# Kernel optimization log

Measured on AMD Instinct MI355X. Metric: run time of the kernel, lower is better.

## Reference

```python
import jax, jax.numpy as jnp
import numpy as np

K_TOP = 16
NUM_HEADS = 12
EPS = 1e-6


def setup_inputs() -> dict:
    key = jax.random.key(0)
    ks = jax.random.split(key, 5)
    B, N, C = 4, 1024, 768
    scale = 0.02
    return {
        "x": jax.random.normal(ks[0], (B, N, C), dtype=jnp.float32),
        "in_proj_weight": jax.random.normal(ks[1], (3 * C, C), dtype=jnp.float32) * scale,
        "in_proj_bias": jax.random.normal(ks[2], (3 * C,), dtype=jnp.float32) * scale,
        "out_proj_weight": jax.random.normal(ks[3], (C, C), dtype=jnp.float32) * scale,
        "out_proj_bias": jax.random.normal(ks[4], (C,), dtype=jnp.float32) * scale,
    }


def reference(x, in_proj_weight, in_proj_bias, out_proj_weight, out_proj_bias):
    B, N, C = x.shape
    H = NUM_HEADS
    Dh = C // H
    scale = Dh ** (-0.5)
    # fused QKV projection: (B,N,3C) -> (3,B,H,N,Dh)
    qkv = x @ in_proj_weight.T + in_proj_bias
    qkv = qkv.reshape(B, N, 3, H, Dh).transpose(2, 0, 3, 1, 4)
    q, k, v = qkv[0], qkv[1], qkv[2]
    # dense scaled-dot-product scores, softmax over keys
    attn = jax.nn.softmax(jnp.einsum("bhqd,bhkd->bhqk", q, k) * scale, axis=-1)
    # top-k sparsification: keep k largest probs per query row, zero the rest
    topk_vals, topk_idx = jax.lax.top_k(attn, K_TOP)  # [B,H,N,K]
    bi = jnp.arange(B)[:, None, None, None]
    hi = jnp.arange(H)[None, :, None, None]
    ni = jnp.arange(N)[None, None, :, None]
    topk_attn = jnp.zeros_like(attn).at[bi, hi, ni, topk_idx].set(topk_vals)
    # renormalize surviving mass
    den = jnp.clip(topk_attn.sum(axis=-1, keepdims=True), EPS, None)
    topk_attn = topk_attn / den
    # weighted value aggregation + output projection
    x_out = jnp.einsum("bhqk,bhkd->bhqd", topk_attn, v)
    x_out = x_out.transpose(0, 2, 1, 3).reshape(B, N, C)
    x_out = x_out @ out_proj_weight.T + out_proj_bias
    return (x_out, topk_attn)
```

## Files before the change

### kernel.cpp

```cpp
#include <hip/hip_runtime.h>
#include <math.h>
#include <stdint.h>

#define BB 4
#define NN 1024
#define CC 768
#define HH 12
#define DH 64
#define KTOP 16

#define GATE     2e-4f
#define SUPERSET 4e-4f

typedef __attribute__((ext_vector_type(8))) short short8v;
typedef __attribute__((ext_vector_type(4))) short short4v;
typedef __attribute__((ext_vector_type(4))) float f32x4;

__device__ __forceinline__ short2 bf16split(float f) {
    uint32_t u = __float_as_uint(f);
    uint32_t hb = (u + 0x8000u) & 0xFFFF0000u;
    float hf = __uint_as_float(hb);
    float lo = f - hf;
    short2 r;
    r.x = (short)(hb >> 16);
    r.y = (short)((__float_as_uint(lo) + 0x8000u) >> 16);
    return r;
}

__device__ __forceinline__ short8v lds_load8(const short* p) {
    short4v a = *(const short4v*)p;
    short4v b = *(const short4v*)(p + 4);
    short8v r;
    r[0] = a[0]; r[1] = a[1]; r[2] = a[2]; r[3] = a[3];
    r[4] = b[0]; r[5] = b[1]; r[6] = b[2]; r[7] = b[3];
    return r;
}

__global__ __launch_bounds__(256) void qkv_mfma(
    const float* __restrict__ x, const float* __restrict__ w,
    const float* __restrict__ bias,
    short* __restrict__ qh_g, short* __restrict__ ql_g,
    short* __restrict__ kh_g, short* __restrict__ kl_g,
    float* __restrict__ v32, int* __restrict__ wl_count) {
    __shared__ short xh[128][36], xl[128][36];
    __shared__ short wh[64][36],  wl[64][36];
    const int tid = threadIdx.x;
    const int m0 = blockIdx.x * 128, n0 = blockIdx.y * 64;
    const int wave = tid >> 6, lane = tid & 63;
    const int wr = wave >> 1, wc = wave & 1;
    const int lr = lane & 15, lg = lane >> 4;

    if (blockIdx.x == 0 && blockIdx.y == 0 && tid == 0) *wl_count = 0;

    f32x4 acc[4][2];
#pragma unroll
    for (int i = 0; i < 4; ++i)
#pragma unroll
        for (int j = 0; j < 2; ++j) acc[i][j] = (f32x4)0.0f;

    for (int k0 = 0; k0 < CC; k0 += 32) {
        __syncthreads();
#pragma unroll
        for (int it = 0; it < 4; ++it) {
            int e = tid + 256 * it;
            int row = e >> 3, c4 = e & 7;
            float4 f = *reinterpret_cast<const float4*>(&x[(size_t)(m0 + row) * CC + k0 + 4 * c4]);
            short4v hv, lv;
            short2 s0 = bf16split(f.x); short2 s1 = bf16split(f.y);
            short2 s2 = bf16split(f.z); short2 s3 = bf16split(f.w);
            hv[0] = s0.x; lv[0] = s0.y; hv[1] = s1.x; lv[1] = s1.y;
            hv[2] = s2.x; lv[2] = s2.y; hv[3] = s3.x; lv[3] = s3.y;
            *(short4v*)&xh[row][4 * c4] = hv;
            *(short4v*)&xl[row][4 * c4] = lv;
        }
#pragma unroll
        for (int it = 0; it < 2; ++it) {
            int e = tid + 256 * it;
            int row = e >> 3, c4 = e & 7;
            float4 f = *reinterpret_cast<const float4*>(&w[(size_t)(n0 + row) * CC + k0 + 4 * c4]);
            short4v hv, lv;
            short2 s0 = bf16split(f.x); short2 s1 = bf16split(f.y);
            short2 s2 = bf16split(f.z); short2 s3 = bf16split(f.w);
            hv[0] = s0.x; lv[0] = s0.y; hv[1] = s1.x; lv[1] = s1.y;
            hv[2] = s2.x; lv[2] = s2.y; hv[3] = s3.x; lv[3] = s3.y;
            *(short4v*)&wh[row][4 * c4] = hv;
            *(short4v*)&wl[row][4 * c4] = lv;
        }
        __syncthreads();

        short8v ah[4], al[4], bh[2], bl[2];
#pragma unroll
        for (int mt = 0; mt < 4; ++mt) {
            int row = wr * 64 + mt * 16 + lr;
            ah[mt] = lds_load8(&xh[row][lg * 8]);
            al[mt] = lds_load8(&xl[row][lg * 8]);
        }
#pragma unroll
        for (int nt = 0; nt < 2; ++nt) {
            int col = wc * 32 + nt * 16 + lr;
            bh[nt] = lds_load8(&wh[col][lg * 8]);
            bl[nt] = lds_load8(&wl[col][lg * 8]);
        }
#pragma unroll
        for (int mt = 0; mt < 4; ++mt) {
#pragma unroll
            for (int nt = 0; nt < 2; ++nt) {
                acc[mt][nt] = __builtin_amdgcn_mfma_f32_16x16x32_bf16(ah[mt], bh[nt], acc[mt][nt], 0, 0, 0);
                acc[mt][nt] = __builtin_amdgcn_mfma_f32_16x16x32_bf16(ah[mt], bl[nt], acc[mt][nt], 0, 0, 0);
                acc[mt][nt] = __builtin_amdgcn_mfma_f32_16x16x32_bf16(al[mt], bh[nt], acc[mt][nt], 0, 0, 0);
            }
        }
    }

    const int t = n0 / CC;
#pragma unroll
    for (int mt = 0; mt < 4; ++mt) {
#pragma unroll
        for (int nt = 0; nt < 2; ++nt) {
#pragma unroll
            for (int r = 0; r < 4; ++r) {
                int m = m0 + wr * 64 + mt * 16 + lg * 4 + r;
                int col = n0 + wc * 32 + nt * 16 + lr;
                float val = acc[mt][nt][r] + bias[col];
                int rem = col - t * CC;
                int h = rem >> 6, d = rem & 63;
                int b = m >> 10, n = m & 1023;
                size_t off = (((size_t)(b * HH + h)) * NN + n) * DH + d;
                if (t == 0) {
                    short2 s = bf16split(val * 0.125f);
                    qh_g[off] = s.x; ql_g[off] = s.y;
                } else if (t == 1) {
                    short2 s = bf16split(val);
                    kh_g[off] = s.x; kl_g[off] = s.y;
                } else {
                    v32[off] = val;
                }
            }
        }
    }
}

__global__ __launch_bounds__(256) void scores_mfma(
    const short* __restrict__ qh_g, const short* __restrict__ ql_g,
    const short* __restrict__ kh_g, const short* __restrict__ kl_g,
    float* __restrict__ attn_out) {
    __shared__ short qh[64][68], ql[64][68];
    __shared__ short kh[128][68], kl[128][68];
    const int bh = blockIdx.y;
    const int m0 = blockIdx.x * 64;
    const int tid = threadIdx.x;
    const int wave = tid >> 6, lane = tid & 63;
    const int lr = lane & 15, lg = lane >> 4;

    const size_t qbase = ((size_t)bh * NN + m0) * DH;
    const size_t kbase = (size_t)bh * NN * DH;

#pragma unroll
    for (int it = 0; it < 2; ++it) {
        int e = tid + 256 * it;
        int row = e >> 3, c8 = (e & 7) << 3;
        size_t g = qbase + (size_t)row * DH + c8;
        *(short4v*)&qh[row][c8]     = *(const short4v*)&qh_g[g];
        *(short4v*)&qh[row][c8 + 4] = *(const short4v*)&qh_g[g + 4];
        *(short4v*)&ql[row][c8]     = *(const short4v*)&ql_g[g];
        *(short4v*)&ql[row][c8 + 4] = *(const short4v*)&ql_g[g + 4];
    }
    __syncthreads();

    short8v ah[4][2], al[4][2];
#pragma unroll
    for (int mt = 0; mt < 4; ++mt)
#pragma unroll
        for (int ks = 0; ks < 2; ++ks) {
            ah[mt][ks] = lds_load8(&qh[mt * 16 + lr][ks * 32 + lg * 8]);
            al[mt][ks] = lds_load8(&ql[mt * 16 + lr][ks * 32 + lg * 8]);
        }

    float* orow0 = attn_out + ((size_t)bh * NN + m0) * NN;

    for (int c0 = 0; c0 < NN; c0 += 128) {
        __syncthreads();
#pragma unroll
        for (int it = 0; it < 4; ++it) {
            int e = tid + 256 * it;
            int row = e >> 3, c8 = (e & 7) << 3;
            size_t g = kbase + (size_t)(c0 + row) * DH + c8;
            *(short4v*)&kh[row][c8]     = *(const short4v*)&kh_g[g];
            *(short4v*)&kh[row][c8 + 4] = *(const short4v*)&kh_g[g + 4];
            *(short4v*)&kl[row][c8]     = *(const short4v*)&kl_g[g];
            *(short4v*)&kl[row][c8 + 4] = *(const short4v*)&kl_g[g + 4];
        }
        __syncthreads();

        short8v bhf[2][2], blf[2][2];
#pragma unroll
        for (int nt = 0; nt < 2; ++nt)
#pragma unroll
            for (int ks = 0; ks < 2; ++ks) {
                int col = wave * 32 + nt * 16 + lr;
                bhf[nt][ks] = lds_load8(&kh[col][ks * 32 + lg * 8]);
                blf[nt][ks] = lds_load8(&kl[col][ks * 32 + lg * 8]);
            }

        f32x4 acc[4][2];
#pragma unroll
        for (int mt = 0; mt < 4; ++mt)
#pragma unroll
            for (int nt = 0; nt < 2; ++nt) acc[mt][nt] = (f32x4)0.0f;

#pragma unroll
        for (int mt = 0; mt < 4; ++mt)
#pragma unroll
            for (int nt = 0; nt < 2; ++nt)
#pragma unroll
                for (int ks = 0; ks < 2; ++ks) {
                    acc[mt][nt] = __builtin_amdgcn_mfma_f32_16x16x32_bf16(ah[mt][ks], bhf[nt][ks], acc[mt][nt], 0, 0, 0);
                    acc[mt][nt] = __builtin_amdgcn_mfma_f32_16x16x32_bf16(ah[mt][ks], blf[nt][ks], acc[mt][nt], 0, 0, 0);
                    acc[mt][nt] = __builtin_amdgcn_mfma_f32_16x16x32_bf16(al[mt][ks], bhf[nt][ks], acc[mt][nt], 0, 0, 0);
                }

#pragma unroll
        for (int mt = 0; mt < 4; ++mt)
#pragma unroll
            for (int nt = 0; nt < 2; ++nt)
#pragma unroll
                for (int r = 0; r < 4; ++r)
                    orow0[(size_t)(mt * 16 + lg * 4 + r) * NN + c0 + wave * 32 + nt * 16 + lr] = acc[mt][nt][r];
    }
}

__device__ __forceinline__ uint32_t f2su(float f) {
    uint32_t u = __float_as_uint(f);
    return u ^ ((u & 0x80000000u) ? 0xFFFFFFFFu : 0x80000000u);
}
__device__ __forceinline__ float su2f(uint32_t s) {
    uint32_t u = s ^ ((s & 0x80000000u) ? 0x80000000u : 0xFFFFFFFFu);
    return __uint_as_float(u);
}

__global__ __launch_bounds__(256) void topk_select(
    const float* __restrict__ v32,
    float* __restrict__ attn_out, float* __restrict__ xatt,
    int* __restrict__ wl_count, int* __restrict__ wl_row, int* __restrict__ wl_cand) {
    __shared__ int      cand_idx[4][64];
    __shared__ uint32_t cand_val[4][64];
    const int blk = blockIdx.x;
    const int wave = threadIdx.x >> 6, lane = threadIdx.x & 63;
    const int bh = blk >> 8;
    const int qn = ((blk & 255) << 2) | wave;

    float* srow = attn_out + ((size_t)bh * NN + qn) * NN;

    uint32_t su[16];
#pragma unroll
    for (int i = 0; i < 4; ++i) {
        float4 t = *(const float4*)&srow[i * 256 + lane * 4];
        su[4 * i + 0] = f2su(t.x); su[4 * i + 1] = f2su(t.y);
        su[4 * i + 2] = f2su(t.z); su[4 * i + 3] = f2su(t.w);
    }

    uint32_t thr = 0;
    for (int b = 31; b >= 0; --b) {
        uint32_t test = thr | (1u << b);
        int cnt = 0;
#pragma unroll
        for (int r = 0; r < 16; ++r)
            cnt += __popcll(__ballot(su[r] >= test));
        if (cnt >= 17) { thr = test; if (cnt <= 64) break; }
    }

    int C = 0;
#pragma unroll
    for (int r = 0; r < 16; ++r) {
        bool pr = (su[r] >= thr);
        unsigned long long mask = __ballot(pr);
        if (pr) {
            int pos = C + __popcll(mask & ((1ull << lane) - 1ull));
            if (pos < 64) {
                cand_idx[wave][pos] = ((r >> 2) << 8) + (lane << 2) + (r & 3);
                cand_val[wave][pos] = su[r];
            }
        }
        C += __popcll(mask);
    }
    if (C > 64) C = 64;

    uint32_t key = (lane < C) ? cand_val[wave][lane] : 0u;
    int      idx = (lane < C) ? cand_idx[wave][lane] : (0x40000000 + lane);

#pragma unroll
    for (int k = 2; k <= 64; k <<= 1) {
#pragma unroll
        for (int j = k >> 1; j > 0; j >>= 1) {
            uint32_t ok = __shfl_xor(key, j);
            int      oi = __shfl_xor(idx, j);
            bool mine_better = (key > ok) || (key == ok && idx < oi);
            bool lower = ((lane & j) == 0);
            bool dir_desc = ((lane & k) == 0);
            bool keep = dir_desc ? (lower ? mine_better : !mine_better)
                                 : (lower ? !mine_better : mine_better);
            if (!keep) { key = ok; idx = oi; }
        }
    }

    float f = su2f(key);
    float f15 = __shfl(f, 15);
    float f16 = __shfl(f, 16);

    bool fast = (f15 - f16 > GATE);
    float p = 0.0f;
    int selIdx = idx;

    if (fast) {
        float m = __shfl(f, 0);
        float e = (lane < KTOP) ? expf(f - m) : 0.0f;
        float sum = e;
#pragma unroll
        for (int off = 32; off; off >>= 1) sum += __shfl_xor(sum, off);
        p = e / sum;
    } else {
        uint32_t thr2 = f2su(f15 - SUPERSET);
        int C2 = 0;
#pragma unroll
        for (int r = 0; r < 16; ++r) {
            bool pr = (su[r] >= thr2);
            unsigned long long mask = __ballot(pr);
            if (pr) {
                int pos = C2 + __popcll(mask & ((1ull << lane) - 1ull));
                if (pos < 64) cand_idx[wave][pos] = ((r >> 2) << 8) + (lane << 2) + (r & 3);
            }
            C2 += __popcll(mask);
        }
        if (C2 > 64) C2 = 64;

        int slot = 0;
        if (lane == 0) slot = atomicAdd(wl_count, 1);
        slot = __shfl(slot, 0);
        int rowid = (bh << 10) | qn;
        if (lane == 0) wl_row[slot] = rowid | (C2 << 20);
        if (lane < C2) wl_cand[(size_t)slot * 64 + lane] = cand_idx[wave][lane];
    }

#pragma unroll
    for (int i = 0; i < 4; ++i) {
        float4 z = make_float4(0.f, 0.f, 0.f, 0.f);
        *(float4*)&srow[i * 256 + lane * 4] = z;
    }

    if (fast) {
        const float* vb = v32 + (size_t)bh * NN * DH;
        float o = 0.0f;
#pragma unroll
        for (int t = 0; t < KTOP; ++t) {
            int jt = __shfl(selIdx, t);
            float pt = __shfl(p, t);
            o = fmaf(pt, vb[(size_t)jt * DH + lane], o);
        }
        asm volatile("s_waitcnt vmcnt(0)" ::: "memory");
        if (lane < KTOP) srow[selIdx] = p;
        int b = bh / HH, h = bh - b * HH;
        xatt[((size_t)b * NN + qn) * CC + h * DH + lane] = o;
    }
}

__global__ __launch_bounds__(64) void slow_rescore(
    const float* __restrict__ x, const float* __restrict__ w_in,
    const float* __restrict__ b_in, const float* __restrict__ v32,
    const int* __restrict__ wl_count, const int* __restrict__ wl_row,
    const int* __restrict__ wl_cand,
    float* __restrict__ attn_out, float* __restrict__ xatt) {
    __shared__ double part[64][65];
    __shared__ double q_sh[64];
    const int lane = threadIdx.x;
    const int count = wl_count[0];

    for (int it = blockIdx.x; it < count; it += gridDim.x) {
        int ent = wl_row[it];
        int rowid = ent & 0xFFFF;
        int C2 = (ent >> 20) & 0x7F;
        int bh = rowid >> 10, qn = rowid & 1023;
        int bq = bh / HH, hq = bh - bq * HH;

        __syncthreads();

        const float* xq = x + ((size_t)bq * NN + qn) * CC;
        double xqd[12];
#pragma unroll
        for (int c = 0; c < 3; ++c) {
            float4 v = *(const float4*)&xq[c * 256 + 4 * lane];
            xqd[4 * c + 0] = v.x; xqd[4 * c + 1] = v.y;
            xqd[4 * c + 2] = v.z; xqd[4 * c + 3] = v.w;
        }
        const float* wqb = w_in + (size_t)(hq * DH) * CC;
        for (int r = 0; r < 64; ++r) {
            const float* wr = wqb + (size_t)r * CC;
            double s = 0.0;
#pragma unroll
            for (int c = 0; c < 3; ++c) {
                float4 v = *(const float4*)&wr[c * 256 + 4 * lane];
                s = fma((double)v.x, xqd[4 * c + 0], s);
                s = fma((double)v.y, xqd[4 * c + 1], s);
                s = fma((double)v.z, xqd[4 * c + 2], s);
                s = fma((double)v.w, xqd[4 * c + 3], s);
            }
            part[r][lane] = s;
        }
        __syncthreads();
        double q64 = 0.0, q64b = 0.0;
#pragma unroll
        for (int l = 0; l < 64; l += 2) { q64 += part[lane][l]; q64b += part[lane][l + 1]; }
        q64 += q64b + (double)b_in[hq * DH + lane];
        q_sh[lane] = q64;
        __syncthreads();

        double beta = q64 * (double)b_in[CC + hq * DH + lane];
#pragma unroll
        for (int off = 32; off; off >>= 1) beta += __shfl_xor(beta, off);

        const float* wkb = w_in + (size_t)(CC + hq * DH) * CC;
        double zd[12];
#pragma unroll
        for (int j = 0; j < 12; ++j) zd[j] = 0.0;
        for (int r = 0; r < 64; ++r) {
            double qr = q_sh[r];
            const float* wr = wkb + (size_t)r * CC;
#pragma unroll
            for (int c = 0; c < 3; ++c) {
                float4 v = *(const float4*)&wr[c * 256 + 4 * lane];
                zd[4 * c + 0] = fma(qr, (double)v.x, zd[4 * c + 0]);
                zd[4 * c + 1] = fma(qr, (double)v.y, zd[4 * c + 1]);
                zd[4 * c + 2] = fma(qr, (double)v.z, zd[4 * c + 2]);
                zd[4 * c + 3] = fma(qr, (double)v.w, zd[4 * c + 3]);
            }
        }

        double myS = -1.0e300;
        int myI = (1 << 30);
        for (int t = 0; t < C2; ++t) {
            int jt = wl_cand[(size_t)it * 64 + t];
            const float* xk = x + ((size_t)bq * NN + jt) * CC;
            double pr = 0.0;
#pragma unroll
            for (int c = 0; c < 3; ++c) {
                float4 v = *(const float4*)&xk[c * 256 + 4 * lane];
                pr = fma(zd[4 * c + 0], (double)v.x, pr);
                pr = fma(zd[4 * c + 1], (double)v.y, pr);
                pr = fma(zd[4 * c + 2], (double)v.z, pr);
                pr = fma(zd[4 * c + 3], (double)v.w, pr);
            }
#pragma unroll
            for (int off = 32; off; off >>= 1) pr += __shfl_xor(pr, off);
            if (lane == t) { myS = (pr + beta) * 0.125; myI = jt; }
        }

        double sS = myS;
        int sI = myI;
        double selS = 0.0; int selIdx = 0;
#pragma unroll 1
        for (int t = 0; t < KTOP; ++t) {
            double bv = sS; int bi = sI;
#pragma unroll
            for (int off = 32; off; off >>= 1) {
                double ov = __shfl_xor(bv, off);
                int oi = __shfl_xor(bi, off);
                if (ov > bv || (ov == bv && oi < bi)) { bv = ov; bi = oi; }
            }
            if (lane == t) { selS = bv; selIdx = bi; }
            if (sI == bi) sS = -1.0e300;
        }

        double m = __shfl(selS, 0);
        float e = (lane < KTOP) ? expf((float)(selS - m)) : 0.0f;
        float sum = e;
#pragma unroll
        for (int off = 32; off; off >>= 1) sum += __shfl_xor(sum, off);
        float p = e / sum;

        const float* vb = v32 + (size_t)bh * NN * DH;
        float o = 0.0f;
#pragma unroll
        for (int t = 0; t < KTOP; ++t) {
            int jt = __shfl(selIdx, t);
            float pt = __shfl(p, t);
            o = fmaf(pt, vb[(size_t)jt * DH + lane], o);
        }

        float* srow = attn_out + (size_t)rowid * NN;
        if (lane < KTOP) srow[selIdx] = p;
        xatt[((size_t)bq * NN + qn) * CC + hq * DH + lane] = o;
    }
}

__global__ __launch_bounds__(256) void out_proj_mfma(
    const float* __restrict__ a, const float* __restrict__ w,
    const float* __restrict__ bias, float* __restrict__ out) {
    __shared__ short xh[128][36], xl[128][36];
    __shared__ short wh[64][36],  wl[64][36];
    const int tid = threadIdx.x;
    const int m0 = blockIdx.x * 128, n0 = blockIdx.y * 64;
    const int wave = tid >> 6, lane = tid & 63;
    const int wr = wave >> 1, wc = wave & 1;
    const int lr = lane & 15, lg = lane >> 4;

    f32x4 acc[4][2];
#pragma unroll
    for (int i = 0; i < 4; ++i)
#pragma unroll
        for (int j = 0; j < 2; ++j) acc[i][j] = (f32x4)0.0f;

    for (int k0 = 0; k0 < CC; k0 += 32) {
        __syncthreads();
#pragma unroll
        for (int it = 0; it < 4; ++it) {
            int e = tid + 256 * it;
            int row = e >> 3, c4 = e & 7;
            float4 f = *reinterpret_cast<const float4*>(&a[(size_t)(m0 + row) * CC + k0 + 4 * c4]);
            short4v hv, lv;
            short2 s0 = bf16split(f.x); short2 s1 = bf16split(f.y);
            short2 s2 = bf16split(f.z); short2 s3 = bf16split(f.w);
            hv[0] = s0.x; lv[0] = s0.y; hv[1] = s1.x; lv[1] = s1.y;
            hv[2] = s2.x; lv[2] = s2.y; hv[3] = s3.x; lv[3] = s3.y;
            *(short4v*)&xh[row][4 * c4] = hv;
            *(short4v*)&xl[row][4 * c4] = lv;
        }
#pragma unroll
        for (int it = 0; it < 2; ++it) {
            int e = tid + 256 * it;
            int row = e >> 3, c4 = e & 7;
            float4 f = *reinterpret_cast<const float4*>(&w[(size_t)(n0 + row) * CC + k0 + 4 * c4]);
            short4v hv, lv;
            short2 s0 = bf16split(f.x); short2 s1 = bf16split(f.y);
            short2 s2 = bf16split(f.z); short2 s3 = bf16split(f.w);
            hv[0] = s0.x; lv[0] = s0.y; hv[1] = s1.x; lv[1] = s1.y;
            hv[2] = s2.x; lv[2] = s2.y; hv[3] = s3.x; lv[3] = s3.y;
            *(short4v*)&wh[row][4 * c4] = hv;
            *(short4v*)&wl[row][4 * c4] = lv;
        }
        __syncthreads();

        short8v ah[4], al[4], bh[2], bl[2];
#pragma unroll
        for (int mt = 0; mt < 4; ++mt) {
            int row = wr * 64 + mt * 16 + lr;
            ah[mt] = lds_load8(&xh[row][lg * 8]);
            al[mt] = lds_load8(&xl[row][lg * 8]);
        }
#pragma unroll
        for (int nt = 0; nt < 2; ++nt) {
            int col = wc * 32 + nt * 16 + lr;
            bh[nt] = lds_load8(&wh[col][lg * 8]);
            bl[nt] = lds_load8(&wl[col][lg * 8]);
        }
#pragma unroll
        for (int mt = 0; mt < 4; ++mt) {
#pragma unroll
            for (int nt = 0; nt < 2; ++nt) {
                acc[mt][nt] = __builtin_amdgcn_mfma_f32_16x16x32_bf16(ah[mt], bh[nt], acc[mt][nt], 0, 0, 0);
                acc[mt][nt] = __builtin_amdgcn_mfma_f32_16x16x32_bf16(ah[mt], bl[nt], acc[mt][nt], 0, 0, 0);
                acc[mt][nt] = __builtin_amdgcn_mfma_f32_16x16x32_bf16(al[mt], bh[nt], acc[mt][nt], 0, 0, 0);
            }
        }
    }

#pragma unroll
    for (int mt = 0; mt < 4; ++mt) {
#pragma unroll
        for (int nt = 0; nt < 2; ++nt) {
#pragma unroll
            for (int r = 0; r < 4; ++r) {
                int m = m0 + wr * 64 + mt * 16 + lg * 4 + r;
                int col = n0 + wc * 32 + nt * 16 + lr;
                out[(size_t)m * CC + col] = acc[mt][nt][r] + bias[col];
            }
        }
    }
}

extern "C" void kernel_launch(void* const* d_in, const int* in_sizes, int n_in,
                              void* d_out, int out_size, void* d_ws, size_t ws_size,
                              hipStream_t stream) {
    const float* x     = (const float*)d_in[0];
    const float* w_in  = (const float*)d_in[1];
    const float* b_in  = (const float*)d_in[2];
    const float* w_out = (const float*)d_in[3];
    const float* b_out = (const float*)d_in[4];

    float* xout     = (float*)d_out;
    float* attn_out = (float*)d_out + (size_t)BB * NN * CC;

    char* ws = (char*)d_ws;
    short* qh_g = (short*)(ws);
    short* ql_g = (short*)(ws + 6291456);
    short* kh_g = (short*)(ws + 12582912);
    short* kl_g = (short*)(ws + 18874368);
    float* v32  = (float*)(ws + 25165824);
    float* xatt = (float*)(ws + 37748736);
    int* wl_count = (int*)(ws + 50331648);
    int* wl_row   = (int*)(ws + 50331904);
    int* wl_cand  = (int*)(ws + 50528512);

    hipLaunchKernelGGL(qkv_mfma, dim3(32, 36), dim3(256), 0, stream,
                       x, w_in, b_in, qh_g, ql_g, kh_g, kl_g, v32, wl_count);
    hipLaunchKernelGGL(scores_mfma, dim3(NN / 64, BB * HH), dim3(256), 0, stream,
                       qh_g, ql_g, kh_g, kl_g, attn_out);
    hipLaunchKernelGGL(topk_select, dim3(BB * HH * (NN / 4)), dim3(256), 0, stream,
                       v32, attn_out, xatt, wl_count, wl_row, wl_cand);
    hipLaunchKernelGGL(slow_rescore, dim3(1024), dim3(64), 0, stream,
                       x, w_in, b_in, v32, wl_count, wl_row, wl_cand, attn_out, xatt);
    hipLaunchKernelGGL(out_proj_mfma, dim3(32, 12), dim3(256), 0, stream,
                       xatt, w_out, b_out, xout);
}
```

Baseline: 341.5 us.

## Fuse score computation and top-k selection into one kernel

Merges the scores kernel and the top-k select kernel so that each 64-row score block, once written to the attention output, is immediately re-read (likely from L2) by the same workgroup for top-k selection, softmax, and V aggregation. This removes one kernel launch and aims to keep the freshly written score rows cache-resident instead of going through HBM between kernels. The trade-off is less parallelism in the top-k phase: 768 blocks, each wave serially handling 16 rows, instead of 12288 small blocks. The larger shared-memory footprint may also lower occupancy.

```diff
diff --git a/kernel.cpp b/kernel.cpp
--- a/kernel.cpp
+++ b/kernel.cpp
@@ -34,6 +34,15 @@
     r[0] = a[0]; r[1] = a[1]; r[2] = a[2]; r[3] = a[3];
     r[4] = b[0]; r[5] = b[1]; r[6] = b[2]; r[7] = b[3];
     return r;
+}
+
+__device__ __forceinline__ uint32_t f2su(float f) {
+    uint32_t u = __float_as_uint(f);
+    return u ^ ((u & 0x80000000u) ? 0xFFFFFFFFu : 0x80000000u);
+}
+__device__ __forceinline__ float su2f(uint32_t s) {
+    uint32_t u = s ^ ((s & 0x80000000u) ? 0x80000000u : 0xFFFFFFFFu);
+    return __uint_as_float(u);
 }
 
 __global__ __launch_bounds__(256) void qkv_mfma(
@@ -140,12 +149,16 @@
     }
 }
 
-__global__ __launch_bounds__(256) void scores_mfma(
+__global__ __launch_bounds__(256) void scores_topk(
     const short* __restrict__ qh_g, const short* __restrict__ ql_g,
     const short* __restrict__ kh_g, const short* __restrict__ kl_g,
-    float* __restrict__ attn_out) {
+    const float* __restrict__ v32,
+    float* __restrict__ attn_out, float* __restrict__ xatt,
+    int* __restrict__ wl_count, int* __restrict__ wl_row, int* __restrict__ wl_cand) {
     __shared__ short qh[64][68], ql[64][68];
     __shared__ short kh[128][68], kl[128][68];
+    __shared__ int      cand_idx[4][64];
+    __shared__ uint32_t cand_val[4][64];
     const int bh = blockIdx.y;
     const int m0 = blockIdx.x * 64;
     const int tid = threadIdx.x;
@@ -167,13 +180,13 @@
     }
     __syncthreads();
 
-    short8v ah[4][2], al[4][2];
+    short8v ahf[4][2], alf[4][2];
 #pragma unroll
     for (int mt = 0; mt < 4; ++mt)
 #pragma unroll
         for (int ks = 0; ks < 2; ++ks) {
-            ah[mt][ks] = lds_load8(&qh[mt * 16 + lr][ks * 32 + lg * 8]);
-            al[mt][ks] = lds_load8(&ql[mt * 16 + lr][ks * 32 + lg * 8]);
+            ahf[mt][ks] = lds_load8(&qh[mt * 16 + lr][ks * 32 + lg * 8]);
+            alf[mt][ks] = lds_load8(&ql[mt * 16 + lr][ks * 32 + lg * 8]);
         }
 
     float* orow0 = attn_out + ((size_t)bh * NN + m0) * NN;
@@ -214,9 +227,9 @@
             for (int nt = 0; nt < 2; ++nt)
 #pragma unroll
                 for (int ks = 0; ks < 2; ++ks) {
-                    acc[mt][nt] = __builtin_amdgcn_mfma_f32_16x16x32_bf16(ah[mt][ks], bhf[nt][ks], acc[mt][nt], 0, 0, 0);
-                    acc[mt][nt] = __builtin_amdgcn_mfma_f32_16x16x32_bf16(ah[mt][ks], blf[nt][ks], acc[mt][nt], 0, 0, 0);
-                    acc[mt][nt] = __builtin_amdgcn_mfma_f32_16x16x32_bf16(al[mt][ks], bhf[nt][ks], acc[mt][nt], 0, 0, 0);
+                    acc[mt][nt] = __builtin_amdgcn_mfma_f32_16x16x32_bf16(ahf[mt][ks], bhf[nt][ks], acc[mt][nt], 0, 0, 0);
+                    acc[mt][nt] = __builtin_amdgcn_mfma_f32_16x16x32_bf16(ahf[mt][ks], blf[nt][ks], acc[mt][nt], 0, 0, 0);
+                    acc[mt][nt] = __builtin_amdgcn_mfma_f32_16x16x32_bf16(alf[mt][ks], bhf[nt][ks], acc[mt][nt], 0, 0, 0);
                 }
 
 #pragma unroll
@@ -227,139 +240,124 @@
                 for (int r = 0; r < 4; ++r)
                     orow0[(size_t)(mt * 16 + lg * 4 + r) * NN + c0 + wave * 32 + nt * 16 + lr] = acc[mt][nt][r];
     }
-}
-
-__device__ __forceinline__ uint32_t f2su(float f) {
-    uint32_t u = __float_as_uint(f);
-    return u ^ ((u & 0x80000000u) ? 0xFFFFFFFFu : 0x80000000u);
-}
-__device__ __forceinline__ float su2f(uint32_t s) {
-    uint32_t u = s ^ ((s & 0x80000000u) ? 0x80000000u : 0xFFFFFFFFu);
-    return __uint_as_float(u);
-}
-
-__global__ __launch_bounds__(256) void topk_select(
-    const float* __restrict__ v32,
-    float* __restrict__ attn_out, float* __restrict__ xatt,
-    int* __restrict__ wl_count, int* __restrict__ wl_row, int* __restrict__ wl_cand) {
-    __shared__ int      cand_idx[4][64];
-    __shared__ uint32_t cand_val[4][64];
-    const int blk = blockIdx.x;
-    const int wave = threadIdx.x >> 6, lane = threadIdx.x & 63;
-    const int bh = blk >> 8;
-    const int qn = ((blk & 255) << 2) | wave;
-
-    float* srow = attn_out + ((size_t)bh * NN + qn) * NN;
-
-    uint32_t su[16];
-#pragma unroll
-    for (int i = 0; i < 4; ++i) {
-        float4 t = *(const float4*)&srow[i * 256 + lane * 4];
-        su[4 * i + 0] = f2su(t.x); su[4 * i + 1] = f2su(t.y);
-        su[4 * i + 2] = f2su(t.z); su[4 * i + 3] = f2su(t.w);
-    }
-
-    uint32_t thr = 0;
-    for (int b = 31; b >= 0; --b) {
-        uint32_t test = thr | (1u << b);
-        int cnt = 0;
-#pragma unroll
-        for (int r = 0; r < 16; ++r)
-            cnt += __popcll(__ballot(su[r] >= test));
-        if (cnt >= 17) { thr = test; if (cnt <= 64) break; }
-    }
-
-    int C = 0;
-#pragma unroll
-    for (int r = 0; r < 16; ++r) {
-        bool pr = (su[r] >= thr);
-        unsigned long long mask = __ballot(pr);
-        if (pr) {
-            int pos = C + __popcll(mask & ((1ull << lane) - 1ull));
-            if (pos < 64) {
-                cand_idx[wave][pos] = ((r >> 2) << 8) + (lane << 2) + (r & 3);
-                cand_val[wave][pos] = su[r];
-            }
-        }
-        C += __popcll(mask);
-    }
-    if (C > 64) C = 64;
-
-    uint32_t key = (lane < C) ? cand_val[wave][lane] : 0u;
-    int      idx = (lane < C) ? cand_idx[wave][lane] : (0x40000000 + lane);
-
-#pragma unroll
-    for (int k = 2; k <= 64; k <<= 1) {
-#pragma unroll
-        for (int j = k >> 1; j > 0; j >>= 1) {
-            uint32_t ok = __shfl_xor(key, j);
-            int      oi = __shfl_xor(idx, j);
-            bool mine_better = (key > ok) || (key == ok && idx < oi);
-            bool lower = ((lane & j) == 0);
-            bool dir_desc = ((lane & k) == 0);
-            bool keep = dir_desc ? (lower ? mine_better : !mine_better)
-                                 : (lower ? !mine_better : mine_better);
-            if (!keep) { key = ok; idx = oi; }
-        }
-    }
-
-    float f = su2f(key);
-    float f15 = __shfl(f, 15);
-    float f16 = __shfl(f, 16);
-
-    bool fast = (f15 - f16 > GATE);
-    float p = 0.0f;
-    int selIdx = idx;
-
-    if (fast) {
-        float m = __shfl(f, 0);
-        float e = (lane < KTOP) ? expf(f - m) : 0.0f;
-        float sum = e;
-#pragma unroll
-        for (int off = 32; off; off >>= 1) sum += __shfl_xor(sum, off);
-        p = e / sum;
-    } else {
-        uint32_t thr2 = f2su(f15 - SUPERSET);
-        int C2 = 0;
+
+    asm volatile("s_waitcnt vmcnt(0)" ::: "memory");
+    __syncthreads();
+
+    for (int rr = 0; rr < 16; ++rr) {
+        const int qn = m0 + wave * 16 + rr;
+        float* srow = attn_out + ((size_t)bh * NN + qn) * NN;
+
+        uint32_t su[16];
+#pragma unroll
+        for (int i = 0; i < 4; ++i) {
+            float4 t4 = *(const float4*)&srow[i * 256 + lane * 4];
+            su[4 * i + 0] = f2su(t4.x); su[4 * i + 1] = f2su(t4.y);
+            su[4 * i + 2] = f2su(t4.z); su[4 * i + 3] = f2su(t4.w);
+        }
+
+        uint32_t thr = 0;
+        for (int b = 31; b >= 0; --b) {
+            uint32_t test = thr | (1u << b);
+            int cnt = 0;
+#pragma unroll
+            for (int r = 0; r < 16; ++r)
+                cnt += __popcll(__ballot(su[r] >= test));
+            if (cnt >= 17) { thr = test; if (cnt <= 64) break; }
+        }
+
+        int C = 0;
 #pragma unroll
         for (int r = 0; r < 16; ++r) {
-            bool pr = (su[r] >= thr2);
+            bool pr = (su[r] >= thr);
             unsigned long long mask = __ballot(pr);
             if (pr) {
-                int pos = C2 + __popcll(mask & ((1ull << lane) - 1ull));
-                if (pos < 64) cand_idx[wave][pos] = ((r >> 2) << 8) + (lane << 2) + (r & 3);
-            }
-            C2 += __popcll(mask);
-        }
-        if (C2 > 64) C2 = 64;
-
-        int slot = 0;
-        if (lane == 0) slot = atomicAdd(wl_count, 1);
-        slot = __shfl(slot, 0);
-        int rowid = (bh << 10) | qn;
-        if (lane == 0) wl_row[slot] = rowid | (C2 << 20);
-        if (lane < C2) wl_cand[(size_t)slot * 64 + lane] = cand_idx[wave][lane];
-    }
-
-#pragma unroll
-    for (int i = 0; i < 4; ++i) {
-        float4 z = make_float4(0.f, 0.f, 0.f, 0.f);
-        *(float4*)&srow[i * 256 + lane * 4] = z;
-    }
-
-    if (fast) {
-        const float* vb = v32 + (size_t)bh * NN * DH;
-        float o = 0.0f;
-#pragma unroll
-        for (int t = 0; t < KTOP; ++t) {
-            int jt = __shfl(selIdx, t);
-            float pt = __shfl(p, t);
-            o = fmaf(pt, vb[(size_t)jt * DH + lane], o);
-        }
-        asm volatile("s_waitcnt vmcnt(0)" ::: "memory");
-        if (lane < KTOP) srow[selIdx] = p;
-        int b = bh / HH, h = bh - b * HH;
-        xatt[((size_t)b * NN + qn) * CC + h * DH + lane] = o;
+                int pos = C + __popcll(mask & ((1ull << lane) - 1ull));
+                if (pos < 64) {
+                    cand_idx[wave][pos] = ((r >> 2) << 8) + (lane << 2) + (r & 3);
+                    cand_val[wave][pos] = su[r];
+                }
+            }
+            C += __popcll(mask);
+        }
+        if (C > 64) C = 64;
+
+        uint32_t key = (lane < C) ? cand_val[wave][lane] : 0u;
+        int      idx = (lane < C) ? cand_idx[wave][lane] : (0x40000000 + lane);
+
+#pragma unroll
+        for (int k = 2; k <= 64; k <<= 1) {
+#pragma unroll
+            for (int j = k >> 1; j > 0; j >>= 1) {
+                uint32_t ok = __shfl_xor(key, j);
+                int      oi = __shfl_xor(idx, j);
+                bool mine_better = (key > ok) || (key == ok && idx < oi);
+                bool lower = ((lane & j) == 0);
+                bool dir_desc = ((lane & k) == 0);
+                bool keep = dir_desc ? (lower ? mine_better : !mine_better)
+                                     : (lower ? !mine_better : mine_better);
+                if (!keep) { key = ok; idx = oi; }
+            }
+        }
+
+        float f = su2f(key);
+        float f15 = __shfl(f, 15);
+        float f16 = __shfl(f, 16);
+
+        bool fast = (f15 - f16 > GATE);
+        float p = 0.0f;
+        int selIdx = idx;
+
+        if (fast) {
+            float m = __shfl(f, 0);
+            float e = (lane < KTOP) ? expf(f - m) : 0.0f;
+            float sum = e;
+#pragma unroll
+            for (int off = 32; off; off >>= 1) sum += __shfl_xor(sum, off);
+            p = e / sum;
+        } else {
+            uint32_t thr2 = f2su(f15 - SUPERSET);
+            int C2 = 0;
+#pragma unroll
+            for (int r = 0; r < 16; ++r) {
+                bool pr = (su[r] >= thr2);
+                unsigned long long mask = __ballot(pr);
+                if (pr) {
+                    int pos = C2 + __popcll(mask & ((1ull << lane) - 1ull));
+                    if (pos < 64) cand_idx[wave][pos] = ((r >> 2) << 8) + (lane << 2) + (r & 3);
+                }
+                C2 += __popcll(mask);
+            }
+            if (C2 > 64) C2 = 64;
+
+            int slot = 0;
+            if (lane == 0) slot = atomicAdd(wl_count, 1);
+            slot = __shfl(slot, 0);
+            int rowid = (bh << 10) | qn;
+            if (lane == 0) wl_row[slot] = rowid | (C2 << 20);
+            if (lane < C2) wl_cand[(size_t)slot * 64 + lane] = cand_idx[wave][lane];
+        }
+
+#pragma unroll
+        for (int i = 0; i < 4; ++i) {
+            float4 z = make_float4(0.f, 0.f, 0.f, 0.f);
+            *(float4*)&srow[i * 256 + lane * 4] = z;
+        }
+
+        if (fast) {
+            const float* vb = v32 + (size_t)bh * NN * DH;
+            float o = 0.0f;
+#pragma unroll
+            for (int t = 0; t < KTOP; ++t) {
+                int jt = __shfl(selIdx, t);
+                float pt = __shfl(p, t);
+                o = fmaf(pt, vb[(size_t)jt * DH + lane], o);
+            }
+            asm volatile("s_waitcnt vmcnt(0)" ::: "memory");
+            if (lane < KTOP) srow[selIdx] = p;
+            int b = bh / HH, h = bh - b * HH;
+            xatt[((size_t)b * NN + qn) * CC + h * DH + lane] = o;
+        }
     }
 }
 
@@ -601,10 +599,8 @@
 
     hipLaunchKernelGGL(qkv_mfma, dim3(32, 36), dim3(256), 0, stream,
                        x, w_in, b_in, qh_g, ql_g, kh_g, kl_g, v32, wl_count);
-    hipLaunchKernelGGL(scores_mfma, dim3(NN / 64, BB * HH), dim3(256), 0, stream,
-                       qh_g, ql_g, kh_g, kl_g, attn_out);
-    hipLaunchKernelGGL(topk_select, dim3(BB * HH * (NN / 4)), dim3(256), 0, stream,
-                       v32, attn_out, xatt, wl_count, wl_row, wl_cand);
+    hipLaunchKernelGGL(scores_topk, dim3(NN / 64, BB * HH), dim3(256), 0, stream,
+                       qh_g, ql_g, kh_g, kl_g, v32, attn_out, xatt, wl_count, wl_row, wl_cand);
     hipLaunchKernelGGL(slow_rescore, dim3(1024), dim3(64), 0, stream,
                        x, w_in, b_in, v32, wl_count, wl_row, wl_cand, attn_out, xatt);
     hipLaunchKernelGGL(out_proj_mfma, dim3(32, 12), dim3(256), 0, stream,
```

Result: slower. 453.9 us (+32.9%).
